# Optimization experiments

Hardware: AMD Instinct MI355X
Metric: run time of the kernel (lower is better)

Reference implementation:

```python
import jax, jax.numpy as jnp
import numpy as np

B, N, E, DIN, DOUT = 8, 4096, 1024, 256, 256
EPS = 1e-8

def setup_inputs() -> dict:
    key = jax.random.key(0)
    k1, k2, k3, k4 = jax.random.split(key, 4)
    x = jax.random.normal(k1, (B, N, DIN), dtype=jnp.float32)
    H = jax.random.uniform(k2, (B, N, E), dtype=jnp.float32)
    weight = jax.random.normal(k3, (DIN, DOUT), dtype=jnp.float32) * (1.0 / np.sqrt(DOUT))
    bias = jax.random.normal(k4, (DOUT,), dtype=jnp.float32) * (1.0 / np.sqrt(DOUT))
    return {"x": x, "hypergraph_matrix": H, "weight": weight, "bias": bias}

def reference(x, hypergraph_matrix, weight, bias):
    H = hypergraph_matrix                      # [B, N, E]
    d_v = jnp.clip(jnp.sum(H, axis=2), EPS)    # node degrees [B, N]
    d_v_inv_sqrt = d_v ** -0.5
    d_e = jnp.clip(jnp.sum(H, axis=1), EPS)    # hyperedge degrees [B, E]
    d_e_inv = 1.0 / d_e
    # D_v^{-1/2} H D_e^{-1}
    step2 = d_v_inv_sqrt[:, :, None] * H * d_e_inv[:, None, :]   # [B, N, E]
    # (D_v^{-1/2} H D_e^{-1} H^T) D_v^{-1/2}  -- original materializes [B, N, N]
    step3 = jnp.einsum('bne,bme->bnm', step2, H)                 # [B, N, N]
    normalized_matrix = step3 * d_v_inv_sqrt[:, None, :]         # [B, N, N]
    support = jnp.einsum('bnd,df->bnf', x, weight)               # X Theta
    out = jnp.einsum('bnm,bmf->bnf', normalized_matrix, support) + bias
    # dropout is identity in eval / deterministic baseline
    return out
```

## Files before the change

### kernel.cpp

```cpp
#include <hip/hip_runtime.h>
#include <hip/hip_bf16.h>

#define BATCH 8
#define NN 4096
#define EE 1024
#define DIN 256
#define DOUT 256
#define EPS 1e-8f

typedef short bf16x8 __attribute__((ext_vector_type(8)));
typedef float f32x4 __attribute__((ext_vector_type(4)));

__device__ __forceinline__ unsigned short f2bf(float f) {
    unsigned u = __float_as_uint(f);
    return (unsigned short)((u + 0x7FFFu + ((u >> 16) & 1u)) >> 16);
}

__device__ __forceinline__ unsigned pk2(float lo, float hi) {
    __hip_bfloat162 h = __float22bfloat162_rn(float2{lo, hi});
    return *(unsigned*)&h;
}
__device__ __forceinline__ bf16x8 pack8(float4 a, float4 b) {
    union { bf16x8 v; unsigned u[4]; } r;
    r.u[0] = pk2(a.x, a.y); r.u[1] = pk2(a.z, a.w);
    r.u[2] = pk2(b.x, b.y); r.u[3] = pk2(b.z, b.w);
    return r.v;
}

__device__ __forceinline__ void g2l16(const void* g, void* l) {
    __builtin_amdgcn_global_load_lds(
        (const __attribute__((address_space(1))) unsigned*)g,
        (__attribute__((address_space(3))) unsigned*)l, 16, 0, 0);
}


template <int LD>
__device__ __forceinline__ void stage_tile(const unsigned short* src, int k0, short* lds, int tid) {
#pragma unroll
    for (int j = 0; j < 2; ++j) {
        int q = tid + j * 256;
        int r = q >> 2;
        int c = (q ^ (r >> 1)) & 3;
        g2l16(src + (size_t)r * LD + k0 + c * 8, (char*)lds + q * 16);
    }
}

__device__ __forceinline__ bf16x8 frag_ld(const short* lds, int r, int c) {
    int off = (r << 6) | (((c ^ (r >> 1)) & 3) << 4);
    return *(const bf16x8*)((const char*)lds + off);
}

template <int LDA, int LDB>
__device__ __forceinline__ void gemm_core(const unsigned short* A, const unsigned short* B,
                                          int kIters, int k0, f32x4 acc[4][4],
                                          short* As, short* Bs) {
    int tid = threadIdx.x, lane = tid & 63, wave = tid >> 6;
    int wm = (wave >> 1) * 64, wn = (wave & 1) * 64;
    int fr = lane & 15, fc = lane >> 4;
    for (int kt = 0; kt < kIters; ++kt) {
        int k = k0 + kt * 32;
        __syncthreads();
        stage_tile<LDA>(A, k, As, tid);
        stage_tile<LDB>(B, k, Bs, tid);
        __syncthreads();
        bf16x8 av[4], bv[4];
#pragma unroll
        for (int i = 0; i < 4; ++i) av[i] = frag_ld(As, wm + i * 16 + fr, fc);
#pragma unroll
        for (int j = 0; j < 4; ++j) bv[j] = frag_ld(Bs, wn + j * 16 + fr, fc);
#pragma unroll
        for (int i = 0; i < 4; ++i)
#pragma unroll
            for (int j = 0; j < 4; ++j)
                acc[i][j] = __builtin_amdgcn_mfma_f32_16x16x32_bf16(av[i], bv[j], acc[i][j], 0, 0, 0);
    }
}


__global__ __launch_bounds__(256) void prep_h2(const float* __restrict__ H,
                                               unsigned short* __restrict__ Hb,
                                               unsigned short* __restrict__ Ht,
                                               float* __restrict__ dv_acc,
                                               float* __restrict__ de_acc) {
    __shared__ float tile[64][65];
    int ns = blockIdx.x, et = blockIdx.y, b = blockIdx.z;
    int e0 = et * 64;
    int t = threadIdx.x;
    int r = t >> 2, cq = (t & 3) * 16;
    int c = t >> 2, q = (t & 3) * 16;
    float de_part = 0.f;
    float4 v0, v1, v2, v3;
    {
        const float* src = H + ((size_t)(b * NN + ns * 512 + r)) * EE + e0 + cq;
        v0 = *(const float4*)(src + 0);
        v1 = *(const float4*)(src + 4);
        v2 = *(const float4*)(src + 8);
        v3 = *(const float4*)(src + 12);
    }
    for (int it = 0; it < 8; ++it) {
        int n0 = ns * 512 + it * 64;
        float rs = v0.x + v0.y + v0.z + v0.w + v1.x + v1.y + v1.z + v1.w +
                   v2.x + v2.y + v2.z + v2.w + v3.x + v3.y + v3.z + v3.w;
        rs += __shfl_down(rs, 2);
        rs += __shfl_down(rs, 1);
        __syncthreads();
        tile[cq + 0][r] = v0.x;  tile[cq + 1][r] = v0.y;  tile[cq + 2][r] = v0.z;  tile[cq + 3][r] = v0.w;
        tile[cq + 4][r] = v1.x;  tile[cq + 5][r] = v1.y;  tile[cq + 6][r] = v1.z;  tile[cq + 7][r] = v1.w;
        tile[cq + 8][r] = v2.x;  tile[cq + 9][r] = v2.y;  tile[cq + 10][r] = v2.z; tile[cq + 11][r] = v2.w;
        tile[cq + 12][r] = v3.x; tile[cq + 13][r] = v3.y; tile[cq + 14][r] = v3.z; tile[cq + 15][r] = v3.w;
        unsigned short* hd = Hb + ((size_t)(b * NN + n0 + r)) * EE + e0 + cq;
        *(bf16x8*)hd = pack8(v0, v1);
        *(bf16x8*)(hd + 8) = pack8(v2, v3);
        if ((t & 3) == 0) atomicAdd(dv_acc + b * NN + n0 + r, rs);
        __syncthreads();
        if (it < 7) {
            const float* src = H + ((size_t)(b * NN + n0 + 64 + r)) * EE + e0 + cq;
            v0 = *(const float4*)(src + 0);
            v1 = *(const float4*)(src + 4);
            v2 = *(const float4*)(src + 8);
            v3 = *(const float4*)(src + 12);
        }
        float w[16];
#pragma unroll
        for (int j = 0; j < 16; ++j) { w[j] = tile[c][q + j]; de_part += w[j]; }
        bf16x8 p0 = pack8(float4{w[0], w[1], w[2], w[3]}, float4{w[4], w[5], w[6], w[7]});
        bf16x8 p1 = pack8(float4{w[8], w[9], w[10], w[11]}, float4{w[12], w[13], w[14], w[15]});
        unsigned short* dst = Ht + ((size_t)(b * EE + e0 + c)) * NN + n0 + q;
        *(bf16x8*)dst = p0; *(bf16x8*)(dst + 8) = p1;
    }
    de_part += __shfl_down(de_part, 2);
    de_part += __shfl_down(de_part, 1);
    if ((t & 3) == 0) atomicAdd(de_acc + b * EE + e0 + c, de_part);
}

__global__ __launch_bounds__(256) void prep_w(const float* __restrict__ W,
                                              unsigned short* __restrict__ Wt) {
    __shared__ float tile[64][65];
    int w = blockIdx.x;
    int k0 = (w >> 2) * 64, f0 = (w & 3) * 64;
    int t = threadIdx.x;
    int r = t >> 2, cq = (t & 3) * 16;
#pragma unroll
    for (int j = 0; j < 16; j += 4) {
        float4 x4 = *(const float4*)(W + (size_t)(k0 + r) * DOUT + f0 + cq + j);
        tile[r][cq + j] = x4.x; tile[r][cq + j + 1] = x4.y;
        tile[r][cq + j + 2] = x4.z; tile[r][cq + j + 3] = x4.w;
    }
    __syncthreads();
    int c = t >> 2, rq = (t & 3) * 16;
    bf16x8 q0, q1;
#pragma unroll
    for (int j = 0; j < 16; ++j) {
        float x = tile[rq + j][c];
        if (j < 8) q0[j] = (short)f2bf(x); else q1[j - 8] = (short)f2bf(x);
    }
    unsigned short* dst = Wt + (size_t)(f0 + c) * DIN + k0 + rq;
    *(bf16x8*)dst = q0; *(bf16x8*)(dst + 8) = q1;
}


__global__ __launch_bounds__(256) void mfma_xw(const float* __restrict__ X,
                                               const unsigned short* __restrict__ Wt,
                                               const float* __restrict__ dv_acc,
                                               unsigned short* __restrict__ Tt) {
    __shared__ short As[128 * 32], Bs[128 * 32];
    int m0 = blockIdx.x * 128, f0 = blockIdx.y * 128;
    const float* Asrc = X + (size_t)m0 * DIN;
    const unsigned short* Bsrc = Wt + (size_t)f0 * DIN;
    int tid = threadIdx.x, lane = tid & 63, wave = tid >> 6;
    int wm = (wave >> 1) * 64, wn = (wave & 1) * 64;
    int fr = lane & 15, fc = lane >> 4;
    int ar = tid >> 1, ah = tid & 1;
    f32x4 acc[4][4] = {};
    for (int kt = 0; kt < DIN / 32; ++kt) {
        int k = kt * 32;
        __syncthreads();
        stage_tile<DIN>(Bsrc, k, Bs, tid);
        const float* s = Asrc + (size_t)ar * DIN + k + ah * 16;
        float4 x0 = *(const float4*)(s + 0);
        float4 x1 = *(const float4*)(s + 4);
        float4 x2 = *(const float4*)(s + 8);
        float4 x3 = *(const float4*)(s + 12);
        bf16x8 p0 = pack8(x0, x1), p1 = pack8(x2, x3);
        int c0 = 2 * ah, c1 = 2 * ah + 1;
        *(bf16x8*)((char*)As + (ar << 6) + (((c0 ^ (ar >> 1)) & 3) << 4)) = p0;
        *(bf16x8*)((char*)As + (ar << 6) + (((c1 ^ (ar >> 1)) & 3) << 4)) = p1;
        __syncthreads();
        bf16x8 av[4], bv[4];
#pragma unroll
        for (int i = 0; i < 4; ++i) av[i] = frag_ld(As, wm + i * 16 + fr, fc);
#pragma unroll
        for (int j = 0; j < 4; ++j) bv[j] = frag_ld(Bs, wn + j * 16 + fr, fc);
#pragma unroll
        for (int i = 0; i < 4; ++i)
#pragma unroll
            for (int j = 0; j < 4; ++j)
                acc[i][j] = __builtin_amdgcn_mfma_f32_16x16x32_bf16(av[i], bv[j], acc[i][j], 0, 0, 0);
    }
    int rg = (lane >> 4) * 4, cl = lane & 15;
    int b = m0 >> 12, nb = m0 & (NN - 1);
#pragma unroll
    for (int i = 0; i < 4; ++i) {
        int rbase = wm + i * 16 + rg;
        float4 dv = *(const float4*)(dv_acc + m0 + rbase);
        float s0 = rsqrtf(fmaxf(dv.x, EPS)), s1 = rsqrtf(fmaxf(dv.y, EPS));
        float s2 = rsqrtf(fmaxf(dv.z, EPS)), s3 = rsqrtf(fmaxf(dv.w, EPS));
#pragma unroll
        for (int j = 0; j < 4; ++j) {
            int f = f0 + wn + j * 16 + cl;
            f32x4 a = acc[i][j];
            ushort4 o = { f2bf(a.x * s0), f2bf(a.y * s1), f2bf(a.z * s2), f2bf(a.w * s3) };
            *(ushort4*)(Tt + (((size_t)b * DOUT + f) << 12) + nb + rbase) = o;
        }
    }
}

__global__ __launch_bounds__(256) void mfma_ht(const unsigned short* __restrict__ Ht,
                                               const unsigned short* __restrict__ Tt,
                                               float* __restrict__ P) {
    __shared__ short As[128 * 32], Bs[128 * 32];
    int e0 = blockIdx.x * 128, f0 = blockIdx.y * 128;
    int b = blockIdx.z >> 1, s = blockIdx.z & 1;
    f32x4 acc[4][4] = {};
    gemm_core<NN, NN>(Ht + ((size_t)b * EE + e0) * NN, Tt + ((size_t)b * DOUT + f0) * NN,
                      2048 / 32, s * 2048, acc, As, Bs);
    int lane = threadIdx.x & 63, wave = threadIdx.x >> 6;
    int wm = (wave >> 1) * 64, wn = (wave & 1) * 64;
    int rg = (lane >> 4) * 4, cl = lane & 15;
    float* Pb = P + (size_t)s * (BATCH * DOUT * EE) + (size_t)b * (DOUT * EE);
#pragma unroll
    for (int i = 0; i < 4; ++i) {
        int e = e0 + wm + i * 16 + rg;
#pragma unroll
        for (int j = 0; j < 4; ++j) {
            int f = f0 + wn + j * 16 + cl;
            *(f32x4*)(Pb + (size_t)f * EE + e) = acc[i][j];
        }
    }
}

__global__ __launch_bounds__(256) void combine_u(const float* __restrict__ P,
                                                 const float* __restrict__ de_acc,
                                                 unsigned short* __restrict__ Ut) {
    const int PS = BATCH * DOUT * EE;
    int idx = (blockIdx.x * 256 + threadIdx.x) * 4;
    f32x4 s = *(const f32x4*)(P + idx);
    s += *(const f32x4*)(P + PS + idx);
    int b = idx >> 18, e = idx & (EE - 1);
    float4 de = *(const float4*)(de_acc + b * EE + e);
    ushort4 o = { f2bf(s.x / fmaxf(de.x, EPS)), f2bf(s.y / fmaxf(de.y, EPS)),
                  f2bf(s.z / fmaxf(de.z, EPS)), f2bf(s.w / fmaxf(de.w, EPS)) };
    *(ushort4*)(Ut + idx) = o;
}

__global__ __launch_bounds__(256) void mfma_hu(const unsigned short* __restrict__ Ut,
                                               const unsigned short* __restrict__ Hb,
                                               const float* __restrict__ dv_acc,
                                               const float* __restrict__ bias,
                                               float* __restrict__ out) {
    __shared__ short As[128 * 32], Bs[128 * 32];
    int f0 = blockIdx.x * 128, n0 = blockIdx.y * 128, b = blockIdx.z;
    f32x4 acc[4][4] = {};
    gemm_core<EE, EE>(Ut + ((size_t)b * DOUT + f0) * EE, Hb + ((size_t)b * NN + n0) * EE,
                      EE / 32, 0, acc, As, Bs);
    int lane = threadIdx.x & 63, wave = threadIdx.x >> 6;
    int wm = (wave >> 1) * 64, wn = (wave & 1) * 64;
    int rg = (lane >> 4) * 4, cl = lane & 15;
    float dvv[4];
#pragma unroll
    for (int j = 0; j < 4; ++j) {
        int n = n0 + wn + j * 16 + cl;
        dvv[j] = rsqrtf(fmaxf(dv_acc[b * NN + n], EPS));
    }
#pragma unroll
    for (int i = 0; i < 4; ++i) {
        int f = f0 + wm + i * 16 + rg;
        float4 bi = *(const float4*)(bias + f);
#pragma unroll
        for (int j = 0; j < 4; ++j) {
            int n = n0 + wn + j * 16 + cl;
            f32x4 a = acc[i][j];
            float4 o = { a.x * dvv[j] + bi.x, a.y * dvv[j] + bi.y,
                         a.z * dvv[j] + bi.z, a.w * dvv[j] + bi.w };
            *(float4*)(out + (((size_t)b * NN + n) << 8) + f) = o;
        }
    }
}


__global__ __launch_bounds__(256) void dv_kernel(const float* __restrict__ H, float* __restrict__ dv_is) {
    int row = blockIdx.x * 4 + (threadIdx.x >> 6);
    int lane = threadIdx.x & 63;
    const float4* p = (const float4*)(H + (size_t)row * EE);
    float s = 0.f;
#pragma unroll
    for (int j = 0; j < 4; ++j) { float4 v = p[j * 64 + lane]; s += v.x + v.y + v.z + v.w; }
#pragma unroll
    for (int off = 32; off; off >>= 1) s += __shfl_down(s, off);
    if (lane == 0) dv_is[row] = rsqrtf(fmaxf(s, EPS));
}
__global__ void zero_kernel(float* __restrict__ p, int n) {
    int i = blockIdx.x * 256 + threadIdx.x;
    if (i < n) p[i] = 0.f;
}
__global__ __launch_bounds__(256) void de_kernel(const float* __restrict__ H, float* __restrict__ de_acc) {
    int b = blockIdx.x >> 4, chunk = blockIdx.x & 15;
    int e = blockIdx.y * 256 + threadIdx.x;
    const float* p = H + ((size_t)b * NN + chunk * 256) * EE + e;
    float s = 0.f;
    for (int n = 0; n < 256; ++n) s += p[(size_t)n * EE];
    atomicAdd(&de_acc[b * EE + e], s);
}
__global__ void de_finalize(float* __restrict__ de) {
    int i = blockIdx.x * 256 + threadIdx.x;
    de[i] = 1.0f / fmaxf(de[i], EPS);
}
__global__ __launch_bounds__(256) void gemm_xw(const float* __restrict__ X, const float* __restrict__ W,
                                               const float* __restrict__ dv_is, float* __restrict__ T) {
    int b = blockIdx.z;
    int m0 = blockIdx.x * 64, f0 = blockIdx.y * 64;
    const float* A = X + (size_t)b * NN * DIN;
    __shared__ float As[16][68];
    __shared__ float Bs[16][68];
    int tid = threadIdx.x;
    int ar = tid >> 2, ac = (tid & 3) << 2;
    int br = tid >> 4, bc = (tid & 15) << 2;
    int r0 = (tid >> 4) << 2, c0 = (tid & 15) << 2;
    float acc[4][4] = {};
    for (int k0 = 0; k0 < DIN; k0 += 16) {
        float4 av = *(const float4*)&A[(size_t)(m0 + ar) * DIN + k0 + ac];
        float4 bv = *(const float4*)&W[(size_t)(k0 + br) * DOUT + f0 + bc];
        __syncthreads();
        As[ac + 0][ar] = av.x; As[ac + 1][ar] = av.y; As[ac + 2][ar] = av.z; As[ac + 3][ar] = av.w;
        *(float4*)&Bs[br][bc] = bv;
        __syncthreads();
#pragma unroll
        for (int k = 0; k < 16; ++k) {
            float4 a4 = *(const float4*)&As[k][r0];
            float4 b4 = *(const float4*)&Bs[k][c0];
            float a[4] = {a4.x, a4.y, a4.z, a4.w};
            float bb[4] = {b4.x, b4.y, b4.z, b4.w};
#pragma unroll
            for (int i = 0; i < 4; ++i)
#pragma unroll
                for (int j = 0; j < 4; ++j) acc[i][j] = fmaf(a[i], bb[j], acc[i][j]);
        }
    }
#pragma unroll
    for (int i = 0; i < 4; ++i) {
        float dv = dv_is[b * NN + m0 + r0 + i];
        float4 o = {dv * acc[i][0], dv * acc[i][1], dv * acc[i][2], dv * acc[i][3]};
        *(float4*)&T[((size_t)b * NN + m0 + r0 + i) * DOUT + f0 + c0] = o;
    }
}
__global__ __launch_bounds__(256) void gemm_ht(const float* __restrict__ H, const float* __restrict__ T,
                                               const float* __restrict__ de_inv, float* __restrict__ U) {
    int b = blockIdx.z;
    int e0 = blockIdx.x * 64, f0 = blockIdx.y * 64;
    const float* Hb = H + (size_t)b * NN * EE;
    const float* Tb = T + (size_t)b * NN * DOUT;
    __shared__ float As[16][68];
    __shared__ float Bs[16][68];
    int tid = threadIdx.x;
    int lr = tid >> 4, lc = (tid & 15) << 2;
    int r0 = (tid >> 4) << 2, c0 = (tid & 15) << 2;
    float acc[4][4] = {};
    for (int n0 = 0; n0 < NN; n0 += 16) {
        float4 av = *(const float4*)&Hb[(size_t)(n0 + lr) * EE + e0 + lc];
        float4 bv = *(const float4*)&Tb[(size_t)(n0 + lr) * DOUT + f0 + lc];
        __syncthreads();
        *(float4*)&As[lr][lc] = av;
        *(float4*)&Bs[lr][lc] = bv;
        __syncthreads();
#pragma unroll
        for (int k = 0; k < 16; ++k) {
            float4 a4 = *(const float4*)&As[k][r0];
            float4 b4 = *(const float4*)&Bs[k][c0];
            float a[4] = {a4.x, a4.y, a4.z, a4.w};
            float bb[4] = {b4.x, b4.y, b4.z, b4.w};
#pragma unroll
            for (int i = 0; i < 4; ++i)
#pragma unroll
                for (int j = 0; j < 4; ++j) acc[i][j] = fmaf(a[i], bb[j], acc[i][j]);
        }
    }
#pragma unroll
    for (int i = 0; i < 4; ++i) {
        float de = de_inv[b * EE + e0 + r0 + i];
        float4 o = {de * acc[i][0], de * acc[i][1], de * acc[i][2], de * acc[i][3]};
        *(float4*)&U[((size_t)b * EE + e0 + r0 + i) * DOUT + f0 + c0] = o;
    }
}
__global__ __launch_bounds__(256) void gemm_hu(const float* __restrict__ H, const float* __restrict__ U,
                                               const float* __restrict__ dv_is, const float* __restrict__ bias,
                                               float* __restrict__ out) {
    int b = blockIdx.z;
    int n0 = blockIdx.x * 64, f0 = blockIdx.y * 64;
    const float* Hb = H + (size_t)b * NN * EE;
    const float* Ub = U + (size_t)b * EE * DOUT;
    __shared__ float As[16][68];
    __shared__ float Bs[16][68];
    int tid = threadIdx.x;
    int ar = tid >> 2, ac = (tid & 3) << 2;
    int br = tid >> 4, bc = (tid & 15) << 2;
    int r0 = (tid >> 4) << 2, c0 = (tid & 15) << 2;
    float acc[4][4] = {};
    for (int k0 = 0; k0 < EE; k0 += 16) {
        float4 av = *(const float4*)&Hb[(size_t)(n0 + ar) * EE + k0 + ac];
        float4 bv = *(const float4*)&Ub[(size_t)(k0 + br) * DOUT + f0 + bc];
        __syncthreads();
        As[ac + 0][ar] = av.x; As[ac + 1][ar] = av.y; As[ac + 2][ar] = av.z; As[ac + 3][ar] = av.w;
        *(float4*)&Bs[br][bc] = bv;
        __syncthreads();
#pragma unroll
        for (int k = 0; k < 16; ++k) {
            float4 a4 = *(const float4*)&As[k][r0];
            float4 b4 = *(const float4*)&Bs[k][c0];
            float a[4] = {a4.x, a4.y, a4.z, a4.w};
            float bb[4] = {b4.x, b4.y, b4.z, b4.w};
#pragma unroll
            for (int i = 0; i < 4; ++i)
#pragma unroll
                for (int j = 0; j < 4; ++j) acc[i][j] = fmaf(a[i], bb[j], acc[i][j]);
        }
    }
    float4 bi = *(const float4*)&bias[f0 + c0];
#pragma unroll
    for (int i = 0; i < 4; ++i) {
        float dv = dv_is[b * NN + n0 + r0 + i];
        float4 o = {dv * acc[i][0] + bi.x, dv * acc[i][1] + bi.y, dv * acc[i][2] + bi.z, dv * acc[i][3] + bi.w};
        *(float4*)&out[((size_t)b * NN + n0 + r0 + i) * DOUT + f0 + c0] = o;
    }
}

extern "C" void kernel_launch(void* const* d_in, const int* in_sizes, int n_in,
                              void* d_out, int out_size, void* d_ws, size_t ws_size,
                              hipStream_t stream) {
    const float* x    = (const float*)d_in[0];
    const float* H    = (const float*)d_in[1];
    const float* W    = (const float*)d_in[2];
    const float* bias = (const float*)d_in[3];
    float* out = (float*)d_out;

    const size_t NEED = (size_t)(BATCH * NN + BATCH * EE + 2 * BATCH * DOUT * EE) * 4 +
                        ((size_t)DIN * DOUT + (size_t)BATCH * DOUT * EE +
                         2 * (size_t)BATCH * NN * EE + (size_t)BATCH * DOUT * NN) * 2;

    if (ws_size >= NEED) {
        float* dv_acc = (float*)d_ws;
        float* de_acc = dv_acc + BATCH * NN;
        float* P      = de_acc + BATCH * EE;
        unsigned short* Wt = (unsigned short*)(P + (size_t)2 * BATCH * DOUT * EE);
        unsigned short* Ut = Wt + DIN * DOUT;
        unsigned short* Hb = Ut + (size_t)BATCH * DOUT * EE;
        unsigned short* Ht = Hb + (size_t)BATCH * NN * EE;
        unsigned short* Tt = Ht + (size_t)BATCH * NN * EE;

        hipMemsetAsync(dv_acc, 0, (size_t)(BATCH * NN + BATCH * EE) * sizeof(float), stream);
        prep_h2<<<dim3(8, 16, 8), 256, 0, stream>>>(H, Hb, Ht, dv_acc, de_acc);
        prep_w<<<16, 256, 0, stream>>>(W, Wt);
        mfma_xw<<<dim3(256, 2), 256, 0, stream>>>(x, Wt, dv_acc, Tt);
        mfma_ht<<<dim3(8, 2, 16), 256, 0, stream>>>(Ht, Tt, P);
        combine_u<<<2048, 256, 0, stream>>>(P, de_acc, Ut);
        mfma_hu<<<dim3(2, 32, 8), 256, 0, stream>>>(Ut, Hb, dv_acc, bias, out);
    } else {
        float* ws = (float*)d_ws;
        float* dv_is = ws;
        float* de    = ws + BATCH * NN;
        float* U     = de + BATCH * EE;
        float* T = out;
        dv_kernel<<<BATCH * NN / 4, 256, 0, stream>>>(H, dv_is);
        zero_kernel<<<(BATCH * EE + 255) / 256, 256, 0, stream>>>(de, BATCH * EE);
        de_kernel<<<dim3(BATCH * 16, EE / 256), 256, 0, stream>>>(H, de);
        de_finalize<<<BATCH * EE / 256, 256, 0, stream>>>(de);
        gemm_xw<<<dim3(NN / 64, DOUT / 64, BATCH), 256, 0, stream>>>(x, W, dv_is, T);
        gemm_ht<<<dim3(EE / 64, DOUT / 64, BATCH), 256, 0, stream>>>(H, T, de, U);
        gemm_hu<<<dim3(NN / 64, DOUT / 64, BATCH), 256, 0, stream>>>(H, U, dv_is, bias, out);
    }
}
```

Baseline: 368.9 us.

## Restructure H prep transpose access pattern and split H^T GEMM K four ways

Rewrites the H prep kernel so each thread handles 8-wide column chunks of two rows 32 apart. This is meant to give better-coalesced global loads and stores for both the bf16 copy and its transpose, with row and column sums reduced by shuffles. The H^T*T GEMM now splits its K dimension into four chunks instead of two, doubling the grid to fill more CUs. The cost is twice as many fp32 partial buffers, written and then re-read by the combine kernel.

```diff
diff --git a/kernel.cpp b/kernel.cpp
--- a/kernel.cpp
+++ b/kernel.cpp
@@ -77,7 +77,7 @@
 }
 
 
-__global__ __launch_bounds__(256) void prep_h2(const float* __restrict__ H,
+__global__ __launch_bounds__(256) void prep_h3(const float* __restrict__ H,
                                                unsigned short* __restrict__ Hb,
                                                unsigned short* __restrict__ Ht,
                                                float* __restrict__ dv_acc,
@@ -86,51 +86,66 @@
     int ns = blockIdx.x, et = blockIdx.y, b = blockIdx.z;
     int e0 = et * 64;
     int t = threadIdx.x;
-    int r = t >> 2, cq = (t & 3) * 16;
-    int c = t >> 2, q = (t & 3) * 16;
-    float de_part = 0.f;
+    int r8 = t >> 3;
+    int c8 = (t & 7) * 8;
+    float deA = 0.f, deB = 0.f;
     float4 v0, v1, v2, v3;
     {
-        const float* src = H + ((size_t)(b * NN + ns * 512 + r)) * EE + e0 + cq;
-        v0 = *(const float4*)(src + 0);
-        v1 = *(const float4*)(src + 4);
-        v2 = *(const float4*)(src + 8);
-        v3 = *(const float4*)(src + 12);
+        const float* s0 = H + ((size_t)(b * NN + ns * 512 + r8)) * EE + e0 + c8;
+        const float* s1 = s0 + (size_t)32 * EE;
+        v0 = *(const float4*)s0; v1 = *(const float4*)(s0 + 4);
+        v2 = *(const float4*)s1; v3 = *(const float4*)(s1 + 4);
     }
     for (int it = 0; it < 8; ++it) {
         int n0 = ns * 512 + it * 64;
-        float rs = v0.x + v0.y + v0.z + v0.w + v1.x + v1.y + v1.z + v1.w +
-                   v2.x + v2.y + v2.z + v2.w + v3.x + v3.y + v3.z + v3.w;
-        rs += __shfl_down(rs, 2);
-        rs += __shfl_down(rs, 1);
-        __syncthreads();
-        tile[cq + 0][r] = v0.x;  tile[cq + 1][r] = v0.y;  tile[cq + 2][r] = v0.z;  tile[cq + 3][r] = v0.w;
-        tile[cq + 4][r] = v1.x;  tile[cq + 5][r] = v1.y;  tile[cq + 6][r] = v1.z;  tile[cq + 7][r] = v1.w;
-        tile[cq + 8][r] = v2.x;  tile[cq + 9][r] = v2.y;  tile[cq + 10][r] = v2.z; tile[cq + 11][r] = v2.w;
-        tile[cq + 12][r] = v3.x; tile[cq + 13][r] = v3.y; tile[cq + 14][r] = v3.z; tile[cq + 15][r] = v3.w;
-        unsigned short* hd = Hb + ((size_t)(b * NN + n0 + r)) * EE + e0 + cq;
-        *(bf16x8*)hd = pack8(v0, v1);
-        *(bf16x8*)(hd + 8) = pack8(v2, v3);
-        if ((t & 3) == 0) atomicAdd(dv_acc + b * NN + n0 + r, rs);
+        float rs0 = v0.x + v0.y + v0.z + v0.w + v1.x + v1.y + v1.z + v1.w;
+        float rs1 = v2.x + v2.y + v2.z + v2.w + v3.x + v3.y + v3.z + v3.w;
+        rs0 += __shfl_down(rs0, 4); rs0 += __shfl_down(rs0, 2); rs0 += __shfl_down(rs0, 1);
+        rs1 += __shfl_down(rs1, 4); rs1 += __shfl_down(rs1, 2); rs1 += __shfl_down(rs1, 1);
+        unsigned short* hb0 = Hb + ((size_t)(b * NN + n0 + r8)) * EE + e0 + c8;
+        *(bf16x8*)hb0 = pack8(v0, v1);
+        *(bf16x8*)(hb0 + (size_t)32 * EE) = pack8(v2, v3);
+        if ((t & 7) == 0) {
+            atomicAdd(dv_acc + b * NN + n0 + r8, rs0);
+            atomicAdd(dv_acc + b * NN + n0 + 32 + r8, rs1);
+        }
+        __syncthreads();
+        tile[c8 + 0][r8] = v0.x; tile[c8 + 1][r8] = v0.y; tile[c8 + 2][r8] = v0.z; tile[c8 + 3][r8] = v0.w;
+        tile[c8 + 4][r8] = v1.x; tile[c8 + 5][r8] = v1.y; tile[c8 + 6][r8] = v1.z; tile[c8 + 7][r8] = v1.w;
+        int r32 = 32 + r8;
+        tile[c8 + 0][r32] = v2.x; tile[c8 + 1][r32] = v2.y; tile[c8 + 2][r32] = v2.z; tile[c8 + 3][r32] = v2.w;
+        tile[c8 + 4][r32] = v3.x; tile[c8 + 5][r32] = v3.y; tile[c8 + 6][r32] = v3.z; tile[c8 + 7][r32] = v3.w;
         __syncthreads();
         if (it < 7) {
-            const float* src = H + ((size_t)(b * NN + n0 + 64 + r)) * EE + e0 + cq;
-            v0 = *(const float4*)(src + 0);
-            v1 = *(const float4*)(src + 4);
-            v2 = *(const float4*)(src + 8);
-            v3 = *(const float4*)(src + 12);
-        }
-        float w[16];
-#pragma unroll
-        for (int j = 0; j < 16; ++j) { w[j] = tile[c][q + j]; de_part += w[j]; }
-        bf16x8 p0 = pack8(float4{w[0], w[1], w[2], w[3]}, float4{w[4], w[5], w[6], w[7]});
-        bf16x8 p1 = pack8(float4{w[8], w[9], w[10], w[11]}, float4{w[12], w[13], w[14], w[15]});
-        unsigned short* dst = Ht + ((size_t)(b * EE + e0 + c)) * NN + n0 + q;
-        *(bf16x8*)dst = p0; *(bf16x8*)(dst + 8) = p1;
-    }
-    de_part += __shfl_down(de_part, 2);
-    de_part += __shfl_down(de_part, 1);
-    if ((t & 3) == 0) atomicAdd(de_acc + b * EE + e0 + c, de_part);
+            const float* s0 = H + ((size_t)(b * NN + n0 + 64 + r8)) * EE + e0 + c8;
+            const float* s1 = s0 + (size_t)32 * EE;
+            v0 = *(const float4*)s0; v1 = *(const float4*)(s0 + 4);
+            v2 = *(const float4*)s1; v3 = *(const float4*)(s1 + 4);
+        }
+        {
+            float w0 = tile[r8][c8 + 0], w1 = tile[r8][c8 + 1], w2 = tile[r8][c8 + 2], w3 = tile[r8][c8 + 3];
+            float w4 = tile[r8][c8 + 4], w5 = tile[r8][c8 + 5], w6 = tile[r8][c8 + 6], w7 = tile[r8][c8 + 7];
+            float s = w0 + w1 + w2 + w3 + w4 + w5 + w6 + w7;
+            s += __shfl_down(s, 4); s += __shfl_down(s, 2); s += __shfl_down(s, 1);
+            deA += s;
+            bf16x8 p = pack8(float4{w0, w1, w2, w3}, float4{w4, w5, w6, w7});
+            *(bf16x8*)(Ht + ((size_t)(b * EE + e0 + r8)) * NN + n0 + c8) = p;
+        }
+        {
+            int c = 32 + r8;
+            float w0 = tile[c][c8 + 0], w1 = tile[c][c8 + 1], w2 = tile[c][c8 + 2], w3 = tile[c][c8 + 3];
+            float w4 = tile[c][c8 + 4], w5 = tile[c][c8 + 5], w6 = tile[c][c8 + 6], w7 = tile[c][c8 + 7];
+            float s = w0 + w1 + w2 + w3 + w4 + w5 + w6 + w7;
+            s += __shfl_down(s, 4); s += __shfl_down(s, 2); s += __shfl_down(s, 1);
+            deB += s;
+            bf16x8 p = pack8(float4{w0, w1, w2, w3}, float4{w4, w5, w6, w7});
+            *(bf16x8*)(Ht + ((size_t)(b * EE + e0 + c)) * NN + n0 + c8) = p;
+        }
+    }
+    if ((t & 7) == 0) {
+        atomicAdd(de_acc + b * EE + e0 + r8, deA);
+        atomicAdd(de_acc + b * EE + e0 + 32 + r8, deB);
+    }
 }
 
 __global__ __launch_bounds__(256) void prep_w(const float* __restrict__ W,
@@ -220,10 +235,10 @@
                                                float* __restrict__ P) {
     __shared__ short As[128 * 32], Bs[128 * 32];
     int e0 = blockIdx.x * 128, f0 = blockIdx.y * 128;
-    int b = blockIdx.z >> 1, s = blockIdx.z & 1;
+    int b = blockIdx.z >> 2, s = blockIdx.z & 3;
     f32x4 acc[4][4] = {};
     gemm_core<NN, NN>(Ht + ((size_t)b * EE + e0) * NN, Tt + ((size_t)b * DOUT + f0) * NN,
-                      2048 / 32, s * 2048, acc, As, Bs);
+                      1024 / 32, s * 1024, acc, As, Bs);
     int lane = threadIdx.x & 63, wave = threadIdx.x >> 6;
     int wm = (wave >> 1) * 64, wn = (wave & 1) * 64;
     int rg = (lane >> 4) * 4, cl = lane & 15;
@@ -246,6 +261,8 @@
     int idx = (blockIdx.x * 256 + threadIdx.x) * 4;
     f32x4 s = *(const f32x4*)(P + idx);
     s += *(const f32x4*)(P + PS + idx);
+    s += *(const f32x4*)(P + 2 * PS + idx);
+    s += *(const f32x4*)(P + 3 * PS + idx);
     int b = idx >> 18, e = idx & (EE - 1);
     float4 de = *(const float4*)(de_acc + b * EE + e);
     ushort4 o = { f2bf(s.x / fmaxf(de.x, EPS)), f2bf(s.y / fmaxf(de.y, EPS)),
@@ -442,7 +459,7 @@
     const float* bias = (const float*)d_in[3];
     float* out = (float*)d_out;
 
-    const size_t NEED = (size_t)(BATCH * NN + BATCH * EE + 2 * BATCH * DOUT * EE) * 4 +
+    const size_t NEED = (size_t)(BATCH * NN + BATCH * EE + 4 * BATCH * DOUT * EE) * 4 +
                         ((size_t)DIN * DOUT + (size_t)BATCH * DOUT * EE +
                          2 * (size_t)BATCH * NN * EE + (size_t)BATCH * DOUT * NN) * 2;
 
@@ -450,17 +467,17 @@
         float* dv_acc = (float*)d_ws;
         float* de_acc = dv_acc + BATCH * NN;
         float* P      = de_acc + BATCH * EE;
-        unsigned short* Wt = (unsigned short*)(P + (size_t)2 * BATCH * DOUT * EE);
+        unsigned short* Wt = (unsigned short*)(P + (size_t)4 * BATCH * DOUT * EE);
         unsigned short* Ut = Wt + DIN * DOUT;
         unsigned short* Hb = Ut + (size_t)BATCH * DOUT * EE;
         unsigned short* Ht = Hb + (size_t)BATCH * NN * EE;
         unsigned short* Tt = Ht + (size_t)BATCH * NN * EE;
 
         hipMemsetAsync(dv_acc, 0, (size_t)(BATCH * NN + BATCH * EE) * sizeof(float), stream);
-        prep_h2<<<dim3(8, 16, 8), 256, 0, stream>>>(H, Hb, Ht, dv_acc, de_acc);
+        prep_h3<<<dim3(8, 16, 8), 256, 0, stream>>>(H, Hb, Ht, dv_acc, de_acc);
         prep_w<<<16, 256, 0, stream>>>(W, Wt);
         mfma_xw<<<dim3(256, 2), 256, 0, stream>>>(x, Wt, dv_acc, Tt);
-        mfma_ht<<<dim3(8, 2, 16), 256, 0, stream>>>(Ht, Tt, P);
+        mfma_ht<<<dim3(8, 2, 32), 256, 0, stream>>>(Ht, Tt, P);
         combine_u<<<2048, 256, 0, stream>>>(P, de_acc, Ut);
         mfma_hu<<<dim3(2, 32, 8), 256, 0, stream>>>(Ut, Hb, dv_acc, bias, out);
     } else {
```

Measured after the change: 358.7 us. 1.03x faster.
